# Performance work log

Measured on AMD Instinct MI355X. Metric: run time of the kernel, lower is better.

## Reference

```python
import jax, jax.numpy as jnp
import numpy as np

D = 1024      # model dim
H = 16        # heads
DH = D // H   # head dim
T = 1024      # input tokens
B = 2         # batch
P = 4         # persistent tokens
WIN = 256     # sliding window
MH = 4 * D    # neural-memory hidden dim
FF = 4 * D    # ffn hidden dim
EPS = 1e-5


def _layernorm(x, g, b):
    m = jnp.mean(x, axis=-1, keepdims=True)
    v = jnp.mean((x - m) ** 2, axis=-1, keepdims=True)
    return (x - m) * jax.lax.rsqrt(v + EPS) * g + b


def setup_inputs() -> dict:
    key = jax.random.key(0)
    ks = jax.random.split(key, 12)
    s = 0.02
    return {
        "x": jax.random.normal(ks[0], (B, T, D), dtype=jnp.float32),
        "pmem": jax.random.normal(ks[1], (P, D), dtype=jnp.float32) * s,
        # neural memory MLP: dim -> MH -> dim (torch Linear convention W:(out,in))
        "mW1": jax.random.normal(ks[2], (MH, D), dtype=jnp.float32) * s,
        "mb1": jnp.zeros((MH,), dtype=jnp.float32),
        "mW2": jax.random.normal(ks[3], (D, MH), dtype=jnp.float32) * s,
        "mb2": jnp.zeros((D,), dtype=jnp.float32),
        "ln1_g": jnp.ones((D,), dtype=jnp.float32),
        "ln1_b": jnp.zeros((D,), dtype=jnp.float32),
        # MHA packed qkv in-proj and out-proj
        "Wqkv": jax.random.normal(ks[4], (3 * D, D), dtype=jnp.float32) * s,
        "bqkv": jnp.zeros((3 * D,), dtype=jnp.float32),
        "Wo": jax.random.normal(ks[5], (D, D), dtype=jnp.float32) * s,
        "bo": jnp.zeros((D,), dtype=jnp.float32),
        "ln2_g": jnp.ones((D,), dtype=jnp.float32),
        "ln2_b": jnp.zeros((D,), dtype=jnp.float32),
        "fW1": jax.random.normal(ks[6], (FF, D), dtype=jnp.float32) * s,
        "fb1": jnp.zeros((FF,), dtype=jnp.float32),
        "fW2": jax.random.normal(ks[7], (D, FF), dtype=jnp.float32) * s,
        "fb2": jnp.zeros((D,), dtype=jnp.float32),
    }


def _forward(x, pmem, mW1, mb1, mW2, mb2, ln1_g, ln1_b, Wqkv, bqkv, Wo, bo,
             ln2_g, ln2_b, fW1, fb1, fW2, fb2):
    Bc, Tc, Dc = x.shape
    # 1. retrieve from neural long-term memory: 2-layer MLP on x
    mem_ctx = jax.nn.relu(jnp.einsum('btd,hd->bth', x, mW1) + mb1)
    mem_ctx = jnp.einsum('bth,dh->btd', mem_ctx, mW2) + mb2
    # 2. concat persistent tokens, retrieved memory, x along sequence
    pers = jnp.broadcast_to(pmem[None], (Bc, P, Dc))
    aug = jnp.concatenate([pers, mem_ctx, x], axis=1)      # (B, L, D)
    L = aug.shape[1]
    # 3. sliding-window causal attention on norm1(aug)
    h = _layernorm(aug, ln1_g, ln1_b)
    qkv = jnp.einsum('bld,ed->ble', h, Wqkv) + bqkv        # (B, L, 3D)
    q, k, v = jnp.split(qkv, 3, axis=-1)
    q = q.reshape(Bc, L, H, DH)
    k = k.reshape(Bc, L, H, DH)
    v = v.reshape(Bc, L, H, DH)
    scale = 1.0 / np.sqrt(DH).astype(np.float32)
    scores = jnp.einsum('bqhd,bkhd->bhqk', q, k) * scale   # (B, H, L, L)
    i = jnp.arange(L)[:, None]
    j = jnp.arange(L)[None, :]
    allowed = (j <= i) & (j > i - WIN)                     # causal sliding window
    scores = jnp.where(allowed[None, None], scores, jnp.float32(-1e30))
    attn = jax.nn.softmax(scores, axis=-1)
    ctx = jnp.einsum('bhqk,bkhd->bqhd', attn, v).reshape(Bc, L, D)
    h_attn = jnp.einsum('bld,ed->ble', ctx, Wo) + bo
    # 4. residual + FFN
    h_res = aug + h_attn
    f = _layernorm(h_res, ln2_g, ln2_b)
    f = jax.nn.gelu(jnp.einsum('bld,fd->blf', f, fW1) + fb1, approximate=False)
    f = jnp.einsum('blf,df->bld', f, fW2) + fb2
    return h_res + f                                       # (B, P+2T, D)


def reference(x, pmem, mW1, mb1, mW2, mb2, ln1_g, ln1_b, Wqkv, bqkv, Wo, bo,
              ln2_g, ln2_b, fW1, fb1, fW2, fb2):
    return _forward(x, pmem, mW1, mb1, mW2, mb2, ln1_g, ln1_b, Wqkv, bqkv,
                    Wo, bo, ln2_g, ln2_b, fW1, fb1, fW2, fb2)
```

## Files before the change

### kernel.cpp

```cpp
#include <hip/hip_runtime.h>
#include <math.h>

#define D_   1024
#define H_   16
#define DH_  64
#define T_   1024
#define B_   2
#define P_   4
#define L_   2052
#define WIN_ 256
#define MH_  4096
#define FF_  4096

typedef __attribute__((ext_vector_type(8))) short bf16x8;
typedef __attribute__((ext_vector_type(4))) float f32x4;
typedef __attribute__((ext_vector_type(8))) unsigned short ush8;

__device__ __forceinline__ unsigned short f2bf(float f) {
  unsigned int u = __builtin_bit_cast(unsigned int, f);
  u += 0x7fffu + ((u >> 16) & 1u);
  return (unsigned short)(u >> 16);
}
__device__ __forceinline__ float bf2f(unsigned short h) {
  unsigned int u = ((unsigned int)h) << 16;
  return __builtin_bit_cast(float, u);
}

__device__ __forceinline__ void gl16(const unsigned short* g, unsigned short* l) {
  __builtin_amdgcn_global_load_lds(
      (const __attribute__((address_space(1))) unsigned int*)g,
      (__attribute__((address_space(3))) unsigned int*)l, 16, 0, 0);
}

__global__ void cvt_bf16_k(const float* __restrict__ in, unsigned short* __restrict__ out, int n) {
  int i = blockIdx.x * blockDim.x + threadIdx.x;
  int e = i * 4;
  if (e >= n) return;
  float4 v = *(const float4*)(in + e);
  ushort4 o;
  o.x = f2bf(v.x); o.y = f2bf(v.y); o.z = f2bf(v.z); o.w = f2bf(v.w);
  *(ushort4*)(out + e) = o;
}

__global__ void concat_k(const float* __restrict__ x, const float* __restrict__ pmem,
                         const float* __restrict__ p0, const float* __restrict__ p1,
                         const float* __restrict__ mb2, float* __restrict__ aug) {
  int i = blockIdx.x * blockDim.x + threadIdx.x;
  if (i >= (B_ * L_ * D_) / 4) return;
  int e = i * 4;
  int d  = e % D_;
  int rl = (e / D_) % L_;
  int b  = e / (D_ * L_);
  float4 v;
  if (rl < P_) {
    v = *(const float4*)(pmem + rl * D_ + d);
  } else if (rl < P_ + T_) {
    size_t idx = (size_t)(b * T_ + (rl - P_)) * D_ + d;
    float4 a0 = *(const float4*)(p0 + idx);
    float4 a1 = *(const float4*)(p1 + idx);
    float4 bb = *(const float4*)(mb2 + d);
    v = make_float4(a0.x + a1.x + bb.x, a0.y + a1.y + bb.y,
                    a0.z + a1.z + bb.z, a0.w + a1.w + bb.w);
  } else {
    v = *(const float4*)(x + (size_t)(b * T_ + (rl - P_ - T_)) * D_ + d);
  }
  *(float4*)(aug + e) = v;
}

__global__ void reduce10_k(const float* __restrict__ p0, const float* __restrict__ p1,
                           const float* __restrict__ hres, const float* __restrict__ fb2,
                           float* __restrict__ out) {
  int i = blockIdx.x * blockDim.x + threadIdx.x;
  if (i >= (B_ * L_ * D_) / 4) return;
  int e = i * 4;
  int d = e % D_;
  float4 a0 = *(const float4*)(p0 + e);
  float4 a1 = *(const float4*)(p1 + e);
  float4 hr = *(const float4*)(hres + e);
  float4 bb = *(const float4*)(fb2 + d);
  float4 v = make_float4(a0.x + a1.x + hr.x + bb.x, a0.y + a1.y + hr.y + bb.y,
                         a0.z + a1.z + hr.z + bb.z, a0.w + a1.w + hr.w + bb.w);
  *(float4*)(out + e) = v;
}

__global__ __launch_bounds__(256)
void layernorm_k(const float* __restrict__ in, const float* __restrict__ g,
                 const float* __restrict__ bb, unsigned short* __restrict__ out) {
  const int row = blockIdx.x;
  const int tid = threadIdx.x;
  const float* xr = in + (size_t)row * D_;
  float4 v = *(const float4*)(xr + tid * 4);
  float s  = v.x + v.y + v.z + v.w;
  float sq = v.x * v.x + v.y * v.y + v.z * v.z + v.w * v.w;
  #pragma unroll
  for (int o = 1; o < 64; o <<= 1) { s += __shfl_xor(s, o); sq += __shfl_xor(sq, o); }
  __shared__ float red[8];
  const int wid = tid >> 6;
  if ((tid & 63) == 0) { red[wid] = s; red[4 + wid] = sq; }
  __syncthreads();
  s  = red[0] + red[1] + red[2] + red[3];
  sq = red[4] + red[5] + red[6] + red[7];
  const float mean = s * (1.0f / D_);
  const float var  = sq * (1.0f / D_) - mean * mean;
  const float inv  = rsqrtf(var + 1e-5f);
  const int c = tid * 4;
  float4 gv = *(const float4*)(g + c);
  float4 bv = *(const float4*)(bb + c);
  unsigned short* dst = out + (size_t)row * D_ + c;
  dst[0] = f2bf((v.x - mean) * inv * gv.x + bv.x);
  dst[1] = f2bf((v.y - mean) * inv * gv.y + bv.y);
  dst[2] = f2bf((v.z - mean) * inv * gv.z + bv.z);
  dst[3] = f2bf((v.w - mean) * inv * gv.w + bv.w);
}

template<int ACT, int OUTBF, int RESID, int WM, int WN, int NWR, int NWC, int KS, int PART>
__global__ __launch_bounds__(KS * NWR * NWC * 64)
void gemm_bt_k(const unsigned short* __restrict__ A,
               const unsigned short* __restrict__ W,
               const float* __restrict__ bias,
               const float* __restrict__ resid,
               void* __restrict__ Cv,
               int M, int N, int K, int ldK, long long zstride) {
  constexpr int NW = NWR * NWC;
  constexpr int BM = NWR * WM * 16;
  constexpr int BN = NWC * WN * 16;
  constexpr int STG = 2 * KS * (BM + BN) * 32 * 2;
  constexpr int RED = (KS > 1) ? BM * BN * 4 : 0;
  constexpr int SBYTES = STG > RED ? STG : RED;
  __shared__ __align__(16) char smem[SBYTES];
  unsigned short* sA = (unsigned short*)smem;
  unsigned short* sB = sA + 2 * KS * BM * 32;

  const int tid  = threadIdx.x;
  const int lane = tid & 63;
  const int wv   = tid >> 6;
  const int grp  = wv / NW;
  const int wg   = wv % NW;
  const int wr   = wg / NWC, wc = wg % NWC;
  const int gm0  = blockIdx.y * BM;
  const int gn0  = blockIdx.x * BN;

  const int KperG = K / KS;
  const int NT    = KperG / 32;
  const int zofs  = PART ? blockIdx.z * K : 0;

  const f32x4 fz = {0.f, 0.f, 0.f, 0.f};
  f32x4 acc[WM][WN];
  #pragma unroll
  for (int i = 0; i < WM; ++i)
    #pragma unroll
    for (int j = 0; j < WN; ++j) acc[i][j] = fz;

  const int srow = lane >> 2;
  const int skc  = (lane & 3) * 8;
  const unsigned short* gA = A + (size_t)(gm0 + srow) * ldK + grp * KperG + zofs + skc;
  const unsigned short* gB = W + (size_t)(gn0 + srow) * ldK + grp * KperG + zofs + skc;

  const int fr = lane & 15;
  const int fk = (lane >> 4) * 8;

  auto stage = [&](int d, int k0) {
    unsigned short* dA = sA + (d * KS + grp) * BM * 32;
    unsigned short* dB = sB + (d * KS + grp) * BN * 32;
    #pragma unroll
    for (int t = 0; t < BM / (NW * 16); ++t) {
      const int rr = wg * 16 + t * NW * 16;
      gl16(gA + (size_t)rr * ldK + k0, dA + rr * 32);
    }
    #pragma unroll
    for (int t = 0; t < BN / (NW * 16); ++t) {
      const int rr = wg * 16 + t * NW * 16;
      gl16(gB + (size_t)rr * ldK + k0, dB + rr * 32);
    }
  };

  stage(0, 0);
  for (int kt = 0; kt < NT; ++kt) {
    __syncthreads();
    if (kt + 1 < NT) stage((kt + 1) & 1, (kt + 1) * 32);
    const int d = kt & 1;
    const unsigned short* lA = sA + (d * KS + grp) * BM * 32;
    const unsigned short* lB = sB + (d * KS + grp) * BN * 32;
    bf16x8 af[WM], bfr[WN];
    #pragma unroll
    for (int i = 0; i < WM; ++i) af[i]  = *(const bf16x8*)&lA[(wr * WM * 16 + i * 16 + fr) * 32 + fk];
    #pragma unroll
    for (int j = 0; j < WN; ++j) bfr[j] = *(const bf16x8*)&lB[(wc * WN * 16 + j * 16 + fr) * 32 + fk];
    #pragma unroll
    for (int i = 0; i < WM; ++i)
      #pragma unroll
      for (int j = 0; j < WN; ++j)
        acc[i][j] = __builtin_amdgcn_mfma_f32_16x16x32_bf16(af[i], bfr[j], acc[i][j], 0, 0, 0);
  }

  if (KS > 1) {
    __syncthreads();
    f32x4* sR = (f32x4*)smem;
    const int tg = tid & (NW * 64 - 1);
    for (int g = 1; g < KS; ++g) {
      if (grp == g) {
        #pragma unroll
        for (int i = 0; i < WM; ++i)
          #pragma unroll
          for (int j = 0; j < WN; ++j) sR[(tg * WM + i) * WN + j] = acc[i][j];
      }
      __syncthreads();
      if (grp == 0) {
        #pragma unroll
        for (int i = 0; i < WM; ++i)
          #pragma unroll
          for (int j = 0; j < WN; ++j) {
            f32x4 t = sR[(tg * WM + i) * WN + j];
            #pragma unroll
            for (int r = 0; r < 4; ++r) acc[i][j][r] += t[r];
          }
      }
      __syncthreads();
    }
    if (grp != 0) return;
  }

  const int rq = (lane >> 4) * 4;
  if (PART) {
    float* Pout = (float*)Cv + (size_t)blockIdx.z * zstride;
    #pragma unroll
    for (int i = 0; i < WM; ++i) {
      #pragma unroll
      for (int j = 0; j < WN; ++j) {
        const int col = gn0 + wc * WN * 16 + j * 16 + fr;
        #pragma unroll
        for (int r = 0; r < 4; ++r) {
          const int row = gm0 + wr * WM * 16 + i * 16 + rq + r;
          if (row < M) Pout[(size_t)row * N + col] = acc[i][j][r];
        }
      }
    }
    return;
  }
  #pragma unroll
  for (int i = 0; i < WM; ++i) {
    #pragma unroll
    for (int j = 0; j < WN; ++j) {
      const int col = gn0 + wc * WN * 16 + j * 16 + fr;
      const float bcol = bias[col];
      #pragma unroll
      for (int r = 0; r < 4; ++r) {
        const int row = gm0 + wr * WM * 16 + i * 16 + rq + r;
        if (row < M) {
          float v = acc[i][j][r] + bcol;
          if (RESID) v += resid[(size_t)row * N + col];
          if (ACT == 1) v = fmaxf(v, 0.f);
          if (ACT == 2) {
            float t = 0.7978845608f * v * (1.0f + 0.044715f * v * v);
            float e = __expf(2.0f * t);
            v = v - __fdividef(v, e + 1.0f);
          }
          if (OUTBF) ((unsigned short*)Cv)[(size_t)row * N + col] = f2bf(v);
          else       ((float*)Cv)[(size_t)row * N + col] = v;
        }
      }
    }
  }
}

__global__ __launch_bounds__(256)
void attn_k(const unsigned short* __restrict__ qkv, unsigned short* __restrict__ ctx) {
  __shared__ unsigned short Kb[64][72];
  __shared__ unsigned short Vt[64][72];
  __shared__ unsigned short Ps[4][16][72];
  const int tid  = threadIdx.x;
  const int lane = tid & 63;
  const int w    = tid >> 6;
  const int l15  = lane & 15;
  const int l4   = lane >> 4;
  const int qb   = blockIdx.x * 64;
  const int h    = blockIdx.y;
  const int b    = blockIdx.z;

  int qrow = qb + w * 16 + l15;
  if (qrow >= L_) qrow = L_ - 1;
  const unsigned short* qp = qkv + ((size_t)(b * L_ + qrow)) * 3072 + h * 64;
  bf16x8 aq0, aq1;
  #pragma unroll
  for (int e = 0; e < 8; ++e) {
    aq0[e] = (short)f2bf(bf2f(qp[l4 * 8 + e]) * 0.125f);
    aq1[e] = (short)f2bf(bf2f(qp[32 + l4 * 8 + e]) * 0.125f);
  }

  const f32x4 fz = {0.f, 0.f, 0.f, 0.f};
  f32x4 acc_o[4];
  #pragma unroll
  for (int j = 0; j < 4; ++j) acc_o[j] = fz;
  float m_[4], ls[4];
  #pragma unroll
  for (int r = 0; r < 4; ++r) { m_[r] = -3.0e38f; ls[r] = 0.f; }

  int k0 = qb - WIN_;
  if (k0 < 0) k0 = 0;

  for (int kb = k0; kb <= qb; kb += 64) {
    #pragma unroll
    for (int c = tid; c < 512; c += 256) {
      const int row = c >> 3;
      const int cc  = (c & 7) * 8;
      const int g   = kb + row;
      ush8 kv8 = {0, 0, 0, 0, 0, 0, 0, 0}, vv8 = kv8;
      if (g < L_) {
        const unsigned short* base = qkv + ((size_t)(b * L_ + g)) * 3072 + h * 64 + cc;
        kv8 = *(const ush8*)(base + 1024);
        vv8 = *(const ush8*)(base + 2048);
      }
      *(ush8*)&Kb[row][cc] = kv8;
      #pragma unroll
      for (int e = 0; e < 8; ++e) Vt[cc + e][row] = vv8[e];
    }
    __syncthreads();

    f32x4 s[4];
    #pragma unroll
    for (int kt = 0; kt < 4; ++kt) {
      bf16x8 bk0 = *(const bf16x8*)&Kb[kt * 16 + l15][l4 * 8];
      bf16x8 bk1 = *(const bf16x8*)&Kb[kt * 16 + l15][32 + l4 * 8];
      f32x4 t = __builtin_amdgcn_mfma_f32_16x16x32_bf16(aq0, bk0, fz, 0, 0, 0);
      s[kt]   = __builtin_amdgcn_mfma_f32_16x16x32_bf16(aq1, bk1, t,  0, 0, 0);
    }

    #pragma unroll
    for (int r = 0; r < 4; ++r) {
      const int qg = qb + w * 16 + l4 * 4 + r;
      float rm = -3.0e38f;
      #pragma unroll
      for (int kt = 0; kt < 4; ++kt) {
        const int kg = kb + kt * 16 + l15;
        const bool ok = (kg <= qg) && (kg + WIN_ > qg);
        rm = fmaxf(rm, ok ? s[kt][r] : -3.0e38f);
      }
      rm = fmaxf(rm, __shfl_xor(rm, 1));
      rm = fmaxf(rm, __shfl_xor(rm, 2));
      rm = fmaxf(rm, __shfl_xor(rm, 4));
      rm = fmaxf(rm, __shfl_xor(rm, 8));
      const float mn = fmaxf(m_[r], rm);
      const float sf = __expf(m_[r] - mn);
      m_[r] = mn;
      float ps = 0.f;
      #pragma unroll
      for (int kt = 0; kt < 4; ++kt) {
        const int kg = kb + kt * 16 + l15;
        const bool ok = (kg <= qg) && (kg + WIN_ > qg);
        const float p = ok ? __expf(s[kt][r] - mn) : 0.f;
        ps += p;
        Ps[w][l4 * 4 + r][kt * 16 + l15] = f2bf(p);
      }
      ps += __shfl_xor(ps, 1);
      ps += __shfl_xor(ps, 2);
      ps += __shfl_xor(ps, 4);
      ps += __shfl_xor(ps, 8);
      ls[r] = ls[r] * sf + ps;
      #pragma unroll
      for (int j = 0; j < 4; ++j) acc_o[j][r] *= sf;
    }

    #pragma unroll
    for (int ks = 0; ks < 2; ++ks) {
      bf16x8 pa = *(const bf16x8*)&Ps[w][l15][ks * 32 + l4 * 8];
      #pragma unroll
      for (int j = 0; j < 4; ++j) {
        bf16x8 vb = *(const bf16x8*)&Vt[j * 16 + l15][ks * 32 + l4 * 8];
        acc_o[j] = __builtin_amdgcn_mfma_f32_16x16x32_bf16(pa, vb, acc_o[j], 0, 0, 0);
      }
    }
    __syncthreads();
  }

  #pragma unroll
  for (int r = 0; r < 4; ++r) {
    const int qg = qb + w * 16 + l4 * 4 + r;
    if (qg < L_) {
      const float inv = 1.0f / ls[r];
      unsigned short* dst = ctx + ((size_t)(b * L_ + qg)) * 1024 + h * 64 + l15;
      #pragma unroll
      for (int j = 0; j < 4; ++j) dst[j * 16] = f2bf(acc_o[j][r] * inv);
    }
  }
}

extern "C" void kernel_launch(void* const* d_in, const int* in_sizes, int n_in,
                              void* d_out, int out_size, void* d_ws, size_t ws_size,
                              hipStream_t stream) {
  (void)in_sizes; (void)n_in; (void)out_size; (void)ws_size;
  const float* x    = (const float*)d_in[0];
  const float* pmem = (const float*)d_in[1];
  const float* mW1  = (const float*)d_in[2];
  const float* mb1  = (const float*)d_in[3];
  const float* mW2  = (const float*)d_in[4];
  const float* mb2  = (const float*)d_in[5];
  const float* ln1g = (const float*)d_in[6];
  const float* ln1b = (const float*)d_in[7];
  const float* Wqkv = (const float*)d_in[8];
  const float* bqkv = (const float*)d_in[9];
  const float* Wo   = (const float*)d_in[10];
  const float* bo   = (const float*)d_in[11];
  const float* ln2g = (const float*)d_in[12];
  const float* ln2b = (const float*)d_in[13];
  const float* fW1  = (const float*)d_in[14];
  const float* fb1  = (const float*)d_in[15];
  const float* fW2  = (const float*)d_in[16];
  const float* fb2  = (const float*)d_in[17];
  float* outp = (float*)d_out;
  char* ws = (char*)d_ws;

  unsigned short* w1b   = (unsigned short*)(ws + 0ull);
  unsigned short* w2b   = (unsigned short*)(ws + 8388608ull);
  unsigned short* wqkvb = (unsigned short*)(ws + 16777216ull);
  unsigned short* wob   = (unsigned short*)(ws + 23068672ull);
  unsigned short* fw1b  = (unsigned short*)(ws + 25165824ull);
  unsigned short* fw2b  = (unsigned short*)(ws + 33554432ull);
  const size_t S = 41943040ull;
  float* aug  = (float*)(ws + S);
  float* hres = (float*)(ws + S + 16809984ull);
  unsigned short* hlnbuf = (unsigned short*)(ws + S + 33619968ull);
  char* R = ws + S + 42270720ull;
  unsigned short* xb   = (unsigned short*)(R);
  unsigned short* h1   = (unsigned short*)(R + 4194304ull);
  unsigned short* qkvb = (unsigned short*)(R);
  unsigned short* f1   = (unsigned short*)(R + 15826944ull);
  unsigned short* hln  = hlnbuf;
  unsigned short* ctxb = hlnbuf;
  unsigned short* hln2 = hlnbuf;
  float* g2p = hres;
  float* g10p = aug;
  const long long Z10 = 8404992LL;

  auto cvt = [&](const float* src, unsigned short* dst, int n) {
    cvt_bf16_k<<<dim3((n / 4 + 255) / 256), dim3(256), 0, stream>>>(src, dst, n);
  };
  cvt(x,    xb,    B_ * T_ * D_);
  cvt(mW1,  w1b,   MH_ * D_);
  cvt(mW2,  w2b,   D_ * MH_);
  cvt(Wqkv, wqkvb, 3 * D_ * D_);
  cvt(Wo,   wob,   D_ * D_);
  cvt(fW1,  fw1b,  FF_ * D_);
  cvt(fW2,  fw2b,  D_ * FF_);

  const int BT = B_ * T_;
  const int BL = B_ * L_;
  const int NE4 = B_ * L_ * D_ / 4;

  gemm_bt_k<1, 1, 0, 4, 4, 2, 4, 1, 0><<<dim3(MH_ / 256, BT / 128), 512, 0, stream>>>(xb, w1b, mb1, nullptr, h1, BT, MH_, D_, D_, 0);
  gemm_bt_k<0, 0, 0, 4, 4, 2, 2, 1, 1><<<dim3(D_ / 128, BT / 128, 2), 256, 0, stream>>>(h1, w2b, nullptr, nullptr, g2p, BT, D_, MH_ / 2, MH_, (long long)BT * D_);
  concat_k<<<dim3((NE4 + 255) / 256), 256, 0, stream>>>(x, pmem, g2p, g2p + (size_t)BT * D_, mb2, aug);
  layernorm_k<<<dim3(BL), 256, 0, stream>>>(aug, ln1g, ln1b, hln);
  gemm_bt_k<0, 1, 0, 4, 4, 2, 4, 1, 0><<<dim3(3 * D_ / 256, (BL + 127) / 128), 512, 0, stream>>>(hln, wqkvb, bqkv, nullptr, qkvb, BL, 3 * D_, D_, D_, 0);
  attn_k<<<dim3((L_ + 63) / 64, H_, B_), 256, 0, stream>>>(qkvb, ctxb);
  gemm_bt_k<0, 0, 1, 2, 4, 4, 1, 1, 0><<<dim3(D_ / 64, (BL + 127) / 128), 256, 0, stream>>>(ctxb, wob, bo, aug, hres, BL, D_, D_, D_, 0);
  layernorm_k<<<dim3(BL), 256, 0, stream>>>(hres, ln2g, ln2b, hln2);
  gemm_bt_k<2, 1, 0, 4, 4, 2, 4, 1, 0><<<dim3(FF_ / 256, (BL + 127) / 128), 512, 0, stream>>>(hln2, fw1b, fb1, nullptr, f1, BL, FF_, D_, D_, 0);
  gemm_bt_k<0, 0, 0, 4, 4, 2, 2, 1, 1><<<dim3(D_ / 128, (BL + 127) / 128, 2), 256, 0, stream>>>(f1, fw2b, nullptr, nullptr, g10p, BL, D_, FF_ / 2, FF_, Z10);
  reduce10_k<<<dim3((NE4 + 255) / 256), 256, 0, stream>>>(g10p, g10p + Z10, hres, fb2, outp);
}
```

Measured before the change: 354.9 us.

## Deepen GEMM prefetch pipeline, batch weight casts, fuse concat with layernorm

The GEMM main loop now prefetches two K-tiles ahead, using explicit vmcnt/lgkmcnt waits and raw barriers so that global-to-LDS loads overlap the MFMA work and fewer full syncs occur per iteration. The seven bf16 conversion launches are merged into a single 2D-grid launch, and the concat kernel is fused with the first layernorm so aug is not re-read. The hand-placed waitcnt values assume a fixed number of outstanding loads per stage, which is fragile, and the fused layernorm computes variance as E[x^2]-mean^2, which is less numerically stable.

```diff
diff --git a/kernel.cpp b/kernel.cpp
--- a/kernel.cpp
+++ b/kernel.cpp
@@ -32,39 +32,77 @@
       (__attribute__((address_space(3))) unsigned int*)l, 16, 0, 0);
 }
 
-__global__ void cvt_bf16_k(const float* __restrict__ in, unsigned short* __restrict__ out, int n) {
-  int i = blockIdx.x * blockDim.x + threadIdx.x;
-  int e = i * 4;
+__global__ __launch_bounds__(256)
+void cvt7_k(const float* s0, unsigned short* d0, int n0,
+            const float* s1, unsigned short* d1, int n1,
+            const float* s2, unsigned short* d2, int n2,
+            const float* s3, unsigned short* d3, int n3,
+            const float* s4, unsigned short* d4, int n4,
+            const float* s5, unsigned short* d5, int n5,
+            const float* s6, unsigned short* d6, int n6) {
+  const float* s; unsigned short* d; int n;
+  switch (blockIdx.y) {
+    case 0: s = s0; d = d0; n = n0; break;
+    case 1: s = s1; d = d1; n = n1; break;
+    case 2: s = s2; d = d2; n = n2; break;
+    case 3: s = s3; d = d3; n = n3; break;
+    case 4: s = s4; d = d4; n = n4; break;
+    case 5: s = s5; d = d5; n = n5; break;
+    default: s = s6; d = d6; n = n6; break;
+  }
+  int e = (blockIdx.x * 256 + threadIdx.x) * 4;
   if (e >= n) return;
-  float4 v = *(const float4*)(in + e);
+  float4 v = *(const float4*)(s + e);
   ushort4 o;
   o.x = f2bf(v.x); o.y = f2bf(v.y); o.z = f2bf(v.z); o.w = f2bf(v.w);
-  *(ushort4*)(out + e) = o;
-}
-
-__global__ void concat_k(const float* __restrict__ x, const float* __restrict__ pmem,
-                         const float* __restrict__ p0, const float* __restrict__ p1,
-                         const float* __restrict__ mb2, float* __restrict__ aug) {
-  int i = blockIdx.x * blockDim.x + threadIdx.x;
-  if (i >= (B_ * L_ * D_) / 4) return;
-  int e = i * 4;
-  int d  = e % D_;
-  int rl = (e / D_) % L_;
-  int b  = e / (D_ * L_);
+  *(ushort4*)(d + e) = o;
+}
+
+__global__ __launch_bounds__(256)
+void concat_ln1_k(const float* __restrict__ x, const float* __restrict__ pmem,
+                  const float* __restrict__ p0, const float* __restrict__ p1,
+                  const float* __restrict__ mb2, const float* __restrict__ g,
+                  const float* __restrict__ bb,
+                  float* __restrict__ aug, unsigned short* __restrict__ hln) {
+  const int row = blockIdx.x;
+  const int rl  = row % L_;
+  const int b   = row / L_;
+  const int tid = threadIdx.x;
+  const int c   = tid * 4;
   float4 v;
   if (rl < P_) {
-    v = *(const float4*)(pmem + rl * D_ + d);
+    v = *(const float4*)(pmem + rl * D_ + c);
   } else if (rl < P_ + T_) {
-    size_t idx = (size_t)(b * T_ + (rl - P_)) * D_ + d;
+    size_t idx = (size_t)(b * T_ + (rl - P_)) * D_ + c;
     float4 a0 = *(const float4*)(p0 + idx);
     float4 a1 = *(const float4*)(p1 + idx);
-    float4 bb = *(const float4*)(mb2 + d);
-    v = make_float4(a0.x + a1.x + bb.x, a0.y + a1.y + bb.y,
-                    a0.z + a1.z + bb.z, a0.w + a1.w + bb.w);
+    float4 bbv = *(const float4*)(mb2 + c);
+    v = make_float4(a0.x + a1.x + bbv.x, a0.y + a1.y + bbv.y,
+                    a0.z + a1.z + bbv.z, a0.w + a1.w + bbv.w);
   } else {
-    v = *(const float4*)(x + (size_t)(b * T_ + (rl - P_ - T_)) * D_ + d);
-  }
-  *(float4*)(aug + e) = v;
+    v = *(const float4*)(x + (size_t)(b * T_ + (rl - P_ - T_)) * D_ + c);
+  }
+  *(float4*)(aug + (size_t)row * D_ + c) = v;
+  float s  = v.x + v.y + v.z + v.w;
+  float sq = v.x * v.x + v.y * v.y + v.z * v.z + v.w * v.w;
+  #pragma unroll
+  for (int o = 1; o < 64; o <<= 1) { s += __shfl_xor(s, o); sq += __shfl_xor(sq, o); }
+  __shared__ float red[8];
+  const int wid = tid >> 6;
+  if ((tid & 63) == 0) { red[wid] = s; red[4 + wid] = sq; }
+  __syncthreads();
+  s  = red[0] + red[1] + red[2] + red[3];
+  sq = red[4] + red[5] + red[6] + red[7];
+  const float mean = s * (1.0f / D_);
+  const float var  = sq * (1.0f / D_) - mean * mean;
+  const float inv  = rsqrtf(var + 1e-5f);
+  float4 gv = *(const float4*)(g + c);
+  float4 bv = *(const float4*)(bb + c);
+  unsigned short* dst = hln + (size_t)row * D_ + c;
+  dst[0] = f2bf((v.x - mean) * inv * gv.x + bv.x);
+  dst[1] = f2bf((v.y - mean) * inv * gv.y + bv.y);
+  dst[2] = f2bf((v.z - mean) * inv * gv.z + bv.z);
+  dst[3] = f2bf((v.w - mean) * inv * gv.w + bv.w);
 }
 
 __global__ void reduce10_k(const float* __restrict__ p0, const float* __restrict__ p1,
@@ -124,6 +162,7 @@
   constexpr int NW = NWR * NWC;
   constexpr int BM = NWR * WM * 16;
   constexpr int BN = NWC * WN * 16;
+  constexpr int LPS = BM / (NW * 16) + BN / (NW * 16);
   constexpr int STG = 2 * KS * (BM + BN) * 32 * 2;
   constexpr int RED = (KS > 1) ? BM * BN * 4 : 0;
   constexpr int SBYTES = STG > RED ? STG : RED;
@@ -174,10 +213,20 @@
     }
   };
 
+  auto wait_lps = [&]() {
+    if constexpr (LPS == 2)      asm volatile("s_waitcnt vmcnt(2)" ::: "memory");
+    else if constexpr (LPS == 3) asm volatile("s_waitcnt vmcnt(3)" ::: "memory");
+    else if constexpr (LPS == 4) asm volatile("s_waitcnt vmcnt(4)" ::: "memory");
+    else                         asm volatile("s_waitcnt vmcnt(0)" ::: "memory");
+  };
+
   stage(0, 0);
+  stage(1, 32);
+  wait_lps();
+  __builtin_amdgcn_s_barrier();
+  asm volatile("" ::: "memory");
+
   for (int kt = 0; kt < NT; ++kt) {
-    __syncthreads();
-    if (kt + 1 < NT) stage((kt + 1) & 1, (kt + 1) * 32);
     const int d = kt & 1;
     const unsigned short* lA = sA + (d * KS + grp) * BM * 32;
     const unsigned short* lB = sB + (d * KS + grp) * BN * 32;
@@ -186,11 +235,21 @@
     for (int i = 0; i < WM; ++i) af[i]  = *(const bf16x8*)&lA[(wr * WM * 16 + i * 16 + fr) * 32 + fk];
     #pragma unroll
     for (int j = 0; j < WN; ++j) bfr[j] = *(const bf16x8*)&lB[(wc * WN * 16 + j * 16 + fr) * 32 + fk];
+    asm volatile("s_waitcnt lgkmcnt(0)" ::: "memory");
+    __builtin_amdgcn_s_barrier();
+    asm volatile("" ::: "memory");
+    if (kt + 2 < NT) stage(d, (kt + 2) * 32);
     #pragma unroll
     for (int i = 0; i < WM; ++i)
       #pragma unroll
       for (int j = 0; j < WN; ++j)
         acc[i][j] = __builtin_amdgcn_mfma_f32_16x16x32_bf16(af[i], bfr[j], acc[i][j], 0, 0, 0);
+    if (kt + 1 < NT) {
+      if (kt + 2 < NT) wait_lps();
+      else asm volatile("s_waitcnt vmcnt(0)" ::: "memory");
+      __builtin_amdgcn_s_barrier();
+      asm volatile("" ::: "memory");
+    }
   }
 
   if (KS > 1) {
@@ -431,25 +490,18 @@
   float* g10p = aug;
   const long long Z10 = 8404992LL;
 
-  auto cvt = [&](const float* src, unsigned short* dst, int n) {
-    cvt_bf16_k<<<dim3((n / 4 + 255) / 256), dim3(256), 0, stream>>>(src, dst, n);
-  };
-  cvt(x,    xb,    B_ * T_ * D_);
-  cvt(mW1,  w1b,   MH_ * D_);
-  cvt(mW2,  w2b,   D_ * MH_);
-  cvt(Wqkv, wqkvb, 3 * D_ * D_);
-  cvt(Wo,   wob,   D_ * D_);
-  cvt(fW1,  fw1b,  FF_ * D_);
-  cvt(fW2,  fw2b,  D_ * FF_);
-
   const int BT = B_ * T_;
   const int BL = B_ * L_;
   const int NE4 = B_ * L_ * D_ / 4;
 
+  cvt7_k<<<dim3((MH_ * D_ / 4 + 255) / 256, 7), 256, 0, stream>>>(
+      x, xb, B_ * T_ * D_,  mW1, w1b, MH_ * D_,  mW2, w2b, D_ * MH_,
+      Wqkv, wqkvb, 3 * D_ * D_,  Wo, wob, D_ * D_,
+      fW1, fw1b, FF_ * D_,  fW2, fw2b, D_ * FF_);
+
   gemm_bt_k<1, 1, 0, 4, 4, 2, 4, 1, 0><<<dim3(MH_ / 256, BT / 128), 512, 0, stream>>>(xb, w1b, mb1, nullptr, h1, BT, MH_, D_, D_, 0);
   gemm_bt_k<0, 0, 0, 4, 4, 2, 2, 1, 1><<<dim3(D_ / 128, BT / 128, 2), 256, 0, stream>>>(h1, w2b, nullptr, nullptr, g2p, BT, D_, MH_ / 2, MH_, (long long)BT * D_);
-  concat_k<<<dim3((NE4 + 255) / 256), 256, 0, stream>>>(x, pmem, g2p, g2p + (size_t)BT * D_, mb2, aug);
-  layernorm_k<<<dim3(BL), 256, 0, stream>>>(aug, ln1g, ln1b, hln);
+  concat_ln1_k<<<dim3(BL), 256, 0, stream>>>(x, pmem, g2p, g2p + (size_t)BT * D_, mb2, ln1g, ln1b, aug, hln);
   gemm_bt_k<0, 1, 0, 4, 4, 2, 4, 1, 0><<<dim3(3 * D_ / 256, (BL + 127) / 128), 512, 0, stream>>>(hln, wqkvb, bqkv, nullptr, qkvb, BL, 3 * D_, D_, D_, 0);
   attn_k<<<dim3((L_ + 63) / 64, H_, B_), 256, 0, stream>>>(qkvb, ctxb);
   gemm_bt_k<0, 0, 1, 2, 4, 4, 1, 1, 0><<<dim3(D_ / 64, (BL + 127) / 128), 256, 0, stream>>>(ctxb, wob, bo, aug, hres, BL, D_, D_, D_, 0);
```

Measured after the change: 351.9 us. No clear change (-0.9%).
